# Performance work log

Hardware: AMD Instinct MI355X
Metric: run time of the kernel (lower is better)

The kernel has to match this reference:

```python
import jax, jax.numpy as jnp
import numpy as np

D_SINGLE = 512
D_PAIR = 128
RANK = 32
EPS = 1e-5


def layer_norm(x, gamma, beta):
    mu = jnp.mean(x, axis=-1, keepdims=True)
    var = jnp.mean(jnp.square(x - mu), axis=-1, keepdims=True)
    return (x - mu) * jax.lax.rsqrt(var + EPS) * gamma + beta


def setup_inputs() -> dict:
    key = jax.random.key(0)
    ks = jax.random.split(key, 12)
    N = 512
    lim_l = 1.0 / np.sqrt(D_SINGLE)
    lim_o = 1.0 / np.sqrt(RANK * RANK)
    return {
        "single_a": jax.random.normal(ks[0], (N, D_SINGLE), dtype=jnp.float32),
        "single_b": jax.random.normal(ks[1], (N, D_SINGLE), dtype=jnp.float32),
        "ln_g": jnp.ones((D_SINGLE,), jnp.float32),
        "ln_b": jnp.zeros((D_SINGLE,), jnp.float32),
        "w_left": jax.random.uniform(ks[2], (RANK, D_SINGLE), jnp.float32, -lim_l, lim_l),
        "b_left": jax.random.uniform(ks[3], (RANK,), jnp.float32, -lim_l, lim_l),
        "w_right": jax.random.uniform(ks[4], (RANK, D_SINGLE), jnp.float32, -lim_l, lim_l),
        "b_right": jax.random.uniform(ks[5], (RANK,), jnp.float32, -lim_l, lim_l),
        "w_out": jax.random.uniform(ks[6], (D_PAIR, RANK * RANK), jnp.float32, -lim_o, lim_o),
        "b_out": jax.random.uniform(ks[7], (D_PAIR,), jnp.float32, -lim_o, lim_o),
        "lno_g": jnp.ones((D_PAIR,), jnp.float32),
        "lno_b": jnp.zeros((D_PAIR,), jnp.float32),
    }


def reference(single_a, single_b, ln_g, ln_b, w_left, b_left, w_right, b_right,
              w_out, b_out, lno_g, lno_b):
    # shared input LayerNorm, then low-rank projections: [N, rank]
    a = layer_norm(single_a, ln_g, ln_b) @ w_left.T + b_left
    b = layer_norm(single_b, ln_g, ln_b) @ w_right.T + b_right
    # out[i,j,p] = sum_{r,s} a[i,r] b[j,s] W[p, r*RANK+s] + bias  (outer product + out_proj)
    w3 = w_out.reshape(D_PAIR, RANK, RANK)  # [p, r, s]
    # precontract W with b, then batched matmul with a (avoids [N,N,rank^2] tensor)
    wb = jnp.einsum('js,prs->jpr', b, w3)       # [N_b, d_pair, rank]
    out = jnp.einsum('ir,jpr->ijp', a, wb) + b_out  # [N_a, N_b, d_pair]
    return layer_norm(out, lno_g, lno_b)
```

## Files before the change

### kernel.cpp

```cpp
#include <hip/hip_runtime.h>
#include <hip/hip_bf16.h>
#include <math.h>

#define D_SINGLE 512
#define D_PAIR   128
#define RANK     32
#define NROW     512
#define EPS      1e-5f

typedef __attribute__((ext_vector_type(8))) short bf16x8;
typedef __attribute__((ext_vector_type(4))) float f32x4;

__global__ __launch_bounds__(256) void k1_ln_proj(
    const float* __restrict__ xa, const float* __restrict__ xb,
    const float* __restrict__ ln_g, const float* __restrict__ ln_b,
    const float* __restrict__ wl, const float* __restrict__ bl,
    const float* __restrict__ wr, const float* __restrict__ br,
    __hip_bfloat16* __restrict__ a_bf, float* __restrict__ b_proj)
{
    const int bid  = blockIdx.x;
    const int row  = bid & (NROW - 1);
    const bool isb = bid >= NROW;
    const float* x    = (isb ? xb : xa) + row * D_SINGLE;
    const float* W    = isb ? wr : wl;
    const float* bias = isb ? br : bl;
    float*           outf = b_proj + row * RANK;
    __hip_bfloat16*  outh = a_bf   + row * RANK;

    __shared__ float xn[D_SINGLE];
    __shared__ float red[8];

    const int t    = threadIdx.x;
    const int wave = t >> 6;
    const int lane = t & 63;

    float x0 = x[t], x1 = x[t + 256];
    float s  = x0 + x1;
    float ss = x0 * x0 + x1 * x1;
    #pragma unroll
    for (int m = 1; m < 64; m <<= 1) {
        s  += __shfl_xor(s, m);
        ss += __shfl_xor(ss, m);
    }
    if (lane == 0) { red[wave] = s; red[4 + wave] = ss; }
    __syncthreads();
    float S    = red[0] + red[1] + red[2] + red[3];
    float SS   = red[4] + red[5] + red[6] + red[7];
    float mean = S * (1.0f / D_SINGLE);
    float var  = SS * (1.0f / D_SINGLE) - mean * mean;
    float rstd = rsqrtf(var + EPS);
    xn[t]       = (x0 - mean) * rstd * ln_g[t]       + ln_b[t];
    xn[t + 256] = (x1 - mean) * rstd * ln_g[t + 256] + ln_b[t + 256];
    __syncthreads();

    #pragma unroll
    for (int q = 0; q < 8; ++q) {
        int r = wave + 4 * q;
        float acc = 0.f;
        #pragma unroll
        for (int tt = 0; tt < 8; ++tt) {
            int k = lane + 64 * tt;
            acc += xn[k] * W[r * D_SINGLE + k];
        }
        #pragma unroll
        for (int m = 1; m < 64; m <<= 1) acc += __shfl_xor(acc, m);
        if (lane == 0) {
            float v = acc + bias[r];
            if (isb) outf[r] = v;
            else     outh[r] = __float2bfloat16(v);
        }
    }
}

__global__ __launch_bounds__(256) void k2_wb(
    const float* __restrict__ bproj, const float* __restrict__ w_out,
    __hip_bfloat16* __restrict__ wb)
{
    const int g = blockIdx.x >> 4;
    const int c = blockIdx.x & 15;
    const int t = threadIdx.x;

    __shared__ float bl[8 * RANK];
    bl[t] = bproj[g * 8 * RANK + t];
    __syncthreads();

    const int pr = c * 256 + t;
    const int p  = pr >> 5;
    const int r  = pr & 31;

    const float4* wrow = reinterpret_cast<const float4*>(w_out + p * (RANK * RANK) + r * RANK);
    float4 w[8];
    #pragma unroll
    for (int q = 0; q < 8; ++q) w[q] = wrow[q];

    #pragma unroll
    for (int jj = 0; jj < 8; ++jj) {
        float acc = 0.f;
        #pragma unroll
        for (int q = 0; q < 8; ++q) {
            acc += bl[jj * 32 + 4 * q + 0] * w[q].x
                 + bl[jj * 32 + 4 * q + 1] * w[q].y
                 + bl[jj * 32 + 4 * q + 2] * w[q].z
                 + bl[jj * 32 + 4 * q + 3] * w[q].w;
        }
        wb[(size_t)(g * 8 + jj) * 4096 + pr] = __float2bfloat16(acc);
    }
}

__global__ __launch_bounds__(256, 4) void k3_mfma(
    const __hip_bfloat16* __restrict__ a_bf, const __hip_bfloat16* __restrict__ wb_bf,
    const float* __restrict__ b_out, const float* __restrict__ lno_g,
    const float* __restrict__ lno_b, float* __restrict__ out)
{
    const int t    = threadIdx.x;
    const int wv   = t >> 6;
    const int lane = t & 63;
    const int g    = lane >> 4;
    const int c    = lane & 15;
    const int jt   = blockIdx.x & 127;
    const int ib   = blockIdx.x >> 7;
    const int j0   = jt * 4;
    const int i0   = ib * 16;
    const int j    = j0 + wv;

    __shared__ __align__(16) float L[16 * 4 * D_PAIR];

    const short* a_s = reinterpret_cast<const short*>(a_bf);
    const short* wbj = reinterpret_cast<const short*>(wb_bf) + (size_t)j * 4096;

    bf16x8 bfrag = *reinterpret_cast<const bf16x8*>(a_s + (i0 + c) * RANK + g * 8);

    f32x4 acc[8];
    #pragma unroll
    for (int tt = 0; tt < 8; ++tt) {
        bf16x8 af  = *reinterpret_cast<const bf16x8*>(wbj + (tt * 16 + c) * RANK + g * 8);
        f32x4  cin = *reinterpret_cast<const f32x4*>(b_out + tt * 16 + g * 4);
        acc[tt] = __builtin_amdgcn_mfma_f32_16x16x32_bf16(af, bfrag, cin, 0, 0, 0);
    }

    float s = 0.f, ss = 0.f;
    #pragma unroll
    for (int tt = 0; tt < 8; ++tt) {
        #pragma unroll
        for (int r = 0; r < 4; ++r) { float v = acc[tt][r]; s += v; ss += v * v; }
    }
    s  += __shfl_xor(s, 16);  ss += __shfl_xor(ss, 16);
    s  += __shfl_xor(s, 32);  ss += __shfl_xor(ss, 32);
    const float mean = s * (1.0f / D_PAIR);
    const float var  = ss * (1.0f / D_PAIR) - mean * mean;
    const float rstd = rsqrtf(var + EPS);

    #pragma unroll
    for (int tt = 0; tt < 8; ++tt) {
        f32x4 gm = *reinterpret_cast<const f32x4*>(lno_g + tt * 16 + g * 4);
        f32x4 bt = *reinterpret_cast<const f32x4*>(lno_b + tt * 16 + g * 4);
        f32x4 o;
        #pragma unroll
        for (int r = 0; r < 4; ++r)
            o[r] = (acc[tt][r] - mean) * rstd * gm[r] + bt[r];
        int off = c * 2048 + wv * 512 + tt * 64 + g * 16;
        off ^= (c & 7) << 4;
        *reinterpret_cast<f32x4*>(reinterpret_cast<char*>(L) + off) = o;
    }
    __syncthreads();

    const int f     = t & 127;
    const int ihalf = t >> 7;
    #pragma unroll
    for (int rnd = 0; rnd < 8; ++rnd) {
        const int i = rnd * 2 + ihalf;
        int off = i * 2048 + f * 16;
        off ^= (i & 7) << 4;
        f32x4 v = *reinterpret_cast<const f32x4*>(reinterpret_cast<const char*>(L) + off);
        float* dst = out + (size_t)(i0 + i) * (NROW * D_PAIR) + j0 * D_PAIR + f * 4;
        __builtin_nontemporal_store(v, reinterpret_cast<f32x4*>(dst));
    }
}

extern "C" void kernel_launch(void* const* d_in, const int* in_sizes, int n_in,
                              void* d_out, int out_size, void* d_ws, size_t ws_size,
                              hipStream_t stream) {
    const float* single_a = (const float*)d_in[0];
    const float* single_b = (const float*)d_in[1];
    const float* ln_g     = (const float*)d_in[2];
    const float* ln_b     = (const float*)d_in[3];
    const float* w_left   = (const float*)d_in[4];
    const float* b_left   = (const float*)d_in[5];
    const float* w_right  = (const float*)d_in[6];
    const float* b_right  = (const float*)d_in[7];
    const float* w_out    = (const float*)d_in[8];
    const float* b_out    = (const float*)d_in[9];
    const float* lno_g    = (const float*)d_in[10];
    const float* lno_b    = (const float*)d_in[11];
    float* out = (float*)d_out;

    float* ws = (float*)d_ws;
    __hip_bfloat16* a_bf   = (__hip_bfloat16*)ws;
    float*          b_proj = ws + 16384;
    __hip_bfloat16* wb_bf  = (__hip_bfloat16*)(ws + 32768);

    k1_ln_proj<<<2 * NROW, 256, 0, stream>>>(single_a, single_b, ln_g, ln_b,
                                             w_left, b_left, w_right, b_right,
                                             a_bf, b_proj);
    k2_wb<<<1024, 256, 0, stream>>>(b_proj, w_out, wb_bf);
    k3_mfma<<<4096, 256, 0, stream>>>(a_bf, wb_bf, b_out, lno_g, lno_b, out);
}
```

Baseline: 45.83 us.

## Fuse LayerNorm projection and W_out precontraction into one kernel

```diff
diff --git a/kernel.cpp b/kernel.cpp
--- a/kernel.cpp
+++ b/kernel.cpp
@@ -11,99 +11,122 @@
 typedef __attribute__((ext_vector_type(8))) short bf16x8;
 typedef __attribute__((ext_vector_type(4))) float f32x4;
 
-__global__ __launch_bounds__(256) void k1_ln_proj(
+__device__ __forceinline__ float dot4(f32x4 a, f32x4 b) {
+    return a.x * b.x + a.y * b.y + a.z * b.z + a.w * b.w;
+}
+
+__global__ __launch_bounds__(512) void k12_fused(
     const float* __restrict__ xa, const float* __restrict__ xb,
     const float* __restrict__ ln_g, const float* __restrict__ ln_b,
-    const float* __restrict__ wl, const float* __restrict__ bl,
-    const float* __restrict__ wr, const float* __restrict__ br,
-    __hip_bfloat16* __restrict__ a_bf, float* __restrict__ b_proj)
+    const float* __restrict__ wl, const float* __restrict__ bL,
+    const float* __restrict__ wr, const float* __restrict__ bR,
+    const float* __restrict__ w_out,
+    __hip_bfloat16* __restrict__ a_bf, __hip_bfloat16* __restrict__ wb)
 {
     const int bid  = blockIdx.x;
-    const int row  = bid & (NROW - 1);
-    const bool isb = bid >= NROW;
-    const float* x    = (isb ? xb : xa) + row * D_SINGLE;
-    const float* W    = isb ? wr : wl;
-    const float* bias = isb ? br : bl;
-    float*           outf = b_proj + row * RANK;
-    __hip_bfloat16*  outh = a_bf   + row * RANK;
-
-    __shared__ float xn[D_SINGLE];
-    __shared__ float red[8];
-
     const int t    = threadIdx.x;
-    const int wave = t >> 6;
+    const int wv   = t >> 6;
     const int lane = t & 63;
 
-    float x0 = x[t], x1 = x[t + 256];
-    float s  = x0 + x1;
-    float ss = x0 * x0 + x1 * x1;
-    #pragma unroll
-    for (int m = 1; m < 64; m <<= 1) {
-        s  += __shfl_xor(s, m);
-        ss += __shfl_xor(ss, m);
-    }
-    if (lane == 0) { red[wave] = s; red[4 + wave] = ss; }
-    __syncthreads();
-    float S    = red[0] + red[1] + red[2] + red[3];
-    float SS   = red[4] + red[5] + red[6] + red[7];
-    float mean = S * (1.0f / D_SINGLE);
-    float var  = SS * (1.0f / D_SINGLE) - mean * mean;
-    float rstd = rsqrtf(var + EPS);
-    xn[t]       = (x0 - mean) * rstd * ln_g[t]       + ln_b[t];
-    xn[t + 256] = (x1 - mean) * rstd * ln_g[t + 256] + ln_b[t + 256];
-    __syncthreads();
-
-    #pragma unroll
-    for (int q = 0; q < 8; ++q) {
-        int r = wave + 4 * q;
+    if (bid < NROW) {
+        __shared__ float xn[D_SINGLE];
+        __shared__ float red[16];
+        const float* x = xa + bid * D_SINGLE;
+
+        float x0 = x[t];
+        float s = x0, ss = x0 * x0;
+        #pragma unroll
+        for (int m = 1; m < 64; m <<= 1) {
+            s  += __shfl_xor(s, m);
+            ss += __shfl_xor(ss, m);
+        }
+        if (lane == 0) { red[wv] = s; red[8 + wv] = ss; }
+        __syncthreads();
+        float S = 0.f, SS = 0.f;
+        #pragma unroll
+        for (int w = 0; w < 8; ++w) { S += red[w]; SS += red[8 + w]; }
+        const float mean = S * (1.0f / D_SINGLE);
+        const float var  = SS * (1.0f / D_SINGLE) - mean * mean;
+        const float rstd = rsqrtf(var + EPS);
+        xn[t] = (x0 - mean) * rstd * ln_g[t] + ln_b[t];
+        __syncthreads();
+
+        #pragma unroll
+        for (int q = 0; q < 4; ++q) {
+            const int r = wv * 4 + q;
+            float acc = 0.f;
+            #pragma unroll
+            for (int tt = 0; tt < 8; ++tt) {
+                const int k = lane + 64 * tt;
+                acc += xn[k] * wl[r * D_SINGLE + k];
+            }
+            #pragma unroll
+            for (int m = 1; m < 64; m <<= 1) acc += __shfl_xor(acc, m);
+            if (lane == 0)
+                a_bf[bid * RANK + r] = __float2bfloat16(acc + bL[r]);
+        }
+    } else {
+        const int bb  = bid - NROW;
+        const int g   = bb >> 1;
+        const int seg = bb & 1;
+
+        __shared__ __align__(16) float xnb[8][D_SINGLE];
+        __shared__ __align__(16) float bl[8 * RANK];
+
+        const int jw = g * 8 + wv;
+        const float* x = xb + jw * D_SINGLE;
+        float v[8];
+        float s = 0.f, ss = 0.f;
+        #pragma unroll
+        for (int k = 0; k < 8; ++k) {
+            v[k] = x[lane + 64 * k];
+            s += v[k]; ss += v[k] * v[k];
+        }
+        #pragma unroll
+        for (int m = 1; m < 64; m <<= 1) {
+            s  += __shfl_xor(s, m);
+            ss += __shfl_xor(ss, m);
+        }
+        const float mean = s * (1.0f / D_SINGLE);
+        const float var  = ss * (1.0f / D_SINGLE) - mean * mean;
+        const float rstd = rsqrtf(var + EPS);
+        #pragma unroll
+        for (int k = 0; k < 8; ++k) {
+            const int e = lane + 64 * k;
+            xnb[wv][e] = (v[k] - mean) * rstd * ln_g[e] + ln_b[e];
+        }
+        __syncthreads();
+
+        const int r    = lane & 31;
+        const int half = lane >> 5;
+        const f32x4* wr4 = reinterpret_cast<const f32x4*>(wr + r * D_SINGLE + half * 256);
+        const f32x4* xv4 = reinterpret_cast<const f32x4*>(&xnb[wv][half * 256]);
         float acc = 0.f;
         #pragma unroll
-        for (int tt = 0; tt < 8; ++tt) {
-            int k = lane + 64 * tt;
-            acc += xn[k] * W[r * D_SINGLE + k];
-        }
-        #pragma unroll
-        for (int m = 1; m < 64; m <<= 1) acc += __shfl_xor(acc, m);
-        if (lane == 0) {
-            float v = acc + bias[r];
-            if (isb) outf[r] = v;
-            else     outh[r] = __float2bfloat16(v);
-        }
-    }
-}
-
-__global__ __launch_bounds__(256) void k2_wb(
-    const float* __restrict__ bproj, const float* __restrict__ w_out,
-    __hip_bfloat16* __restrict__ wb)
-{
-    const int g = blockIdx.x >> 4;
-    const int c = blockIdx.x & 15;
-    const int t = threadIdx.x;
-
-    __shared__ float bl[8 * RANK];
-    bl[t] = bproj[g * 8 * RANK + t];
-    __syncthreads();
-
-    const int pr = c * 256 + t;
-    const int p  = pr >> 5;
-    const int r  = pr & 31;
-
-    const float4* wrow = reinterpret_cast<const float4*>(w_out + p * (RANK * RANK) + r * RANK);
-    float4 w[8];
-    #pragma unroll
-    for (int q = 0; q < 8; ++q) w[q] = wrow[q];
-
-    #pragma unroll
-    for (int jj = 0; jj < 8; ++jj) {
-        float acc = 0.f;
-        #pragma unroll
-        for (int q = 0; q < 8; ++q) {
-            acc += bl[jj * 32 + 4 * q + 0] * w[q].x
-                 + bl[jj * 32 + 4 * q + 1] * w[q].y
-                 + bl[jj * 32 + 4 * q + 2] * w[q].z
-                 + bl[jj * 32 + 4 * q + 3] * w[q].w;
-        }
-        wb[(size_t)(g * 8 + jj) * 4096 + pr] = __float2bfloat16(acc);
+        for (int k4 = 0; k4 < 64; ++k4)
+            acc += dot4(wr4[k4], xv4[k4]);
+        acc += __shfl_xor(acc, 32);
+        if (half == 0) bl[wv * 32 + r] = acc + bR[r];
+        __syncthreads();
+
+        const f32x4* bl4 = reinterpret_cast<const f32x4*>(bl);
+        #pragma unroll
+        for (int it = 0; it < 4; ++it) {
+            const int pr = (seg * 4 + it) * 512 + t;
+            const int p  = pr >> 5;
+            const int rr = pr & 31;
+            const f32x4* wrow = reinterpret_cast<const f32x4*>(w_out + p * (RANK * RANK) + rr * RANK);
+            f32x4 w8[8];
+            #pragma unroll
+            for (int q = 0; q < 8; ++q) w8[q] = wrow[q];
+            #pragma unroll
+            for (int jj = 0; jj < 8; ++jj) {
+                float a2 = 0.f;
+                #pragma unroll
+                for (int q = 0; q < 8; ++q) a2 += dot4(w8[q], bl4[jj * 8 + q]);
+                wb[(size_t)(g * 8 + jj) * 4096 + pr] = __float2bfloat16(a2);
+            }
+        }
     }
 }
 
@@ -195,13 +218,11 @@
     float* out = (float*)d_out;
 
     float* ws = (float*)d_ws;
-    __hip_bfloat16* a_bf   = (__hip_bfloat16*)ws;
-    float*          b_proj = ws + 16384;
-    __hip_bfloat16* wb_bf  = (__hip_bfloat16*)(ws + 32768);
-
-    k1_ln_proj<<<2 * NROW, 256, 0, stream>>>(single_a, single_b, ln_g, ln_b,
-                                             w_left, b_left, w_right, b_right,
-                                             a_bf, b_proj);
-    k2_wb<<<1024, 256, 0, stream>>>(b_proj, w_out, wb_bf);
+    __hip_bfloat16* a_bf  = (__hip_bfloat16*)ws;
+    __hip_bfloat16* wb_bf = (__hip_bfloat16*)(ws + 32768);
+
+    k12_fused<<<NROW + 128, 512, 0, stream>>>(single_a, single_b, ln_g, ln_b,
+                                              w_left, b_left, w_right, b_right,
+                                              w_out, a_bf, wb_bf);
     k3_mfma<<<4096, 256, 0, stream>>>(a_bf, wb_bf, b_out, lno_g, lno_b, out);
 }
```

New measurement: 59.82 us. 30.5% more time.
